# Optimization experiments

Measured on AMD Instinct MI355X. Metric: run time of the kernel, lower is better.

Reference implementation:

```python
import jax, jax.numpy as jnp
import numpy as np

B, N1, N2 = 4, 2048, 8192
F_IN, F_OUT = 256, 256
K = 3          # PyG knn_interpolate default
BN_EPS = 1e-5


def linear_bn(x, W, b, gamma, beta):
    # Linear + BatchNorm1d (training mode: batch stats over B*N per feature)
    h = jnp.einsum('bni,io->bno', x, W) + b
    mean = h.mean(axis=(0, 1))
    var = h.var(axis=(0, 1))
    xhat = (h - mean) * jax.lax.rsqrt(var + BN_EPS)
    return gamma * xhat + beta


def knn_interpolate(f1, p1, p2):
    # f1: [N1,F], p1: [N1,3], p2: [N2,3] -> [N2,F]
    d2 = jnp.sum((p2[:, None, :] - p1[None, :, :]) ** 2, axis=-1)  # [N2,N1]
    neg_d2, idx = jax.lax.top_k(-d2, K)                            # k smallest
    w = 1.0 / jnp.maximum(-neg_d2, 1e-16)                          # [N2,K]
    fk = f1[idx]                                                   # [N2,K,F]
    return jnp.sum(w[..., None] * fk, axis=1) / jnp.sum(w, axis=1, keepdims=True)


def setup_inputs() -> dict:
    key = jax.random.key(0)
    ks = jax.random.split(key, 10)
    return {
        'features_1': jax.random.normal(ks[0], (B, N1, F_IN), jnp.float32),
        'positions_1': jax.random.uniform(ks[1], (B, N1, 3), jnp.float32),
        'batch_1': jnp.repeat(jnp.arange(B, dtype=jnp.int64), N1),
        'features_2': jax.random.normal(ks[2], (B, N2, F_IN), jnp.float32),
        'positions_2': jax.random.uniform(ks[3], (B, N2, 3), jnp.float32),
        'batch_2': jnp.repeat(jnp.arange(B, dtype=jnp.int64), N2),
        'W1': jax.random.normal(ks[4], (F_IN, F_OUT), jnp.float32) * (1.0 / np.sqrt(F_IN)),
        'b1': jax.random.normal(ks[5], (F_OUT,), jnp.float32) * 0.02,
        'gamma1': jnp.ones((F_OUT,), jnp.float32),
        'beta1': jnp.zeros((F_OUT,), jnp.float32),
        'W2': jax.random.normal(ks[6], (F_IN, F_OUT), jnp.float32) * (1.0 / np.sqrt(F_IN)),
        'b2': jax.random.normal(ks[7], (F_OUT,), jnp.float32) * 0.02,
        'gamma2': jnp.ones((F_OUT,), jnp.float32),
        'beta2': jnp.zeros((F_OUT,), jnp.float32),
    }


def reference(features_1, positions_1, batch_1, features_2, positions_2, batch_2,
              W1, b1, gamma1, beta1, W2, b2, gamma2, beta2):
    f1 = linear_bn(features_1, W1, b1, gamma1, beta1)          # [B,N1,F_OUT]
    f2 = linear_bn(features_2, W2, b2, gamma2, beta2)          # [B,N2,F_OUT]
    # batch structure is regular [B,N]: knn restricted within batch == vmap over B
    interp = jax.vmap(knn_interpolate)(f1, positions_1, positions_2)  # [B,N2,F_OUT]
    return (interp + f2, positions_2, batch_2)
```

## Files before the change

### kernel.cpp

```cpp
#include <hip/hip_runtime.h>
#include <math.h>

#define BATCH   4
#define N1      2048
#define N2      8192
#define F       256
#define NTOT1   (BATCH * N1)
#define NTOT2   (BATCH * N2)
#define BN_EPS  1e-5f

typedef __attribute__((ext_vector_type(8))) short bf16x8;
typedef __attribute__((ext_vector_type(4))) float f32x4;

__device__ __forceinline__ unsigned short f2bf(float f) {
    unsigned u = __float_as_uint(f);
    unsigned r = (u + 0x7fffu + ((u >> 16) & 1u)) >> 16;
    return (unsigned short)r;
}
__device__ __forceinline__ float bf2f(unsigned short u) {
    return __uint_as_float((unsigned)u << 16);
}
__device__ __forceinline__ void async16(const void* g, void* l) {
    __builtin_amdgcn_global_load_lds(
        (const __attribute__((address_space(1))) unsigned int*)g,
        (__attribute__((address_space(3))) unsigned int*)l, 16, 0, 0);
}
__device__ __forceinline__ void ins3b(float d, int j,
                                      float& d0, float& d1, float& d2,
                                      int& j0, int& j1, int& j2) {
    const bool c0 = d < d0;
    const bool c1 = d < d1;
    const bool c2 = d < d2;
    d2 = c1 ? d1 : (c2 ? d : d2);
    j2 = c1 ? j1 : (c2 ? j : j2);
    d1 = c0 ? d0 : (c1 ? d : d1);
    j1 = c0 ? j0 : (c1 ? j : j1);
    d0 = c0 ? d  : d0;
    j0 = c0 ? j  : j0;
}

__global__ __launch_bounds__(256) void prep_kernel(const float4* __restrict__ f1,
                                                   const float4* __restrict__ f2,
                                                   const float* __restrict__ W1,
                                                   const float* __restrict__ W2,
                                                   ushort4* __restrict__ Xb1,
                                                   ushort4* __restrict__ Xb2,
                                                   unsigned short* __restrict__ Wt1,
                                                   unsigned short* __restrict__ Wt2,
                                                   float* __restrict__ sums) {
    const int bx = blockIdx.x;
    const int t  = threadIdx.x;

    if (bx < 8192) {
        const int i = bx * 256 + t;
        const float4 v = f2[i];
        ushort4 o;
        o.x = f2bf(v.x); o.y = f2bf(v.y); o.z = f2bf(v.z); o.w = f2bf(v.w);
        Xb2[i] = o;
    } else if (bx < 10240) {
        const int i = (bx - 8192) * 256 + t;
        const float4 v = f1[i];
        ushort4 o;
        o.x = f2bf(v.x); o.y = f2bf(v.y); o.z = f2bf(v.z); o.w = f2bf(v.w);
        Xb1[i] = o;
    } else if (bx < 10272) {
        __shared__ float tile[64][65];
        const int bb = bx - 10240;
        const bool second = bb >= 16;
        const int bl = second ? bb - 16 : bb;
        const float* W = second ? W2 : W1;
        unsigned short* Wt = second ? Wt2 : Wt1;
        const int gx0 = (bl & 3) * 64;
        const int gy0 = (bl >> 2) * 64;
        const int tx = t & 63;
        const int ty = t >> 6;
        #pragma unroll
        for (int j = 0; j < 16; ++j) {
            const int row = ty * 16 + j;
            tile[row][tx] = W[(size_t)(gy0 + row) * 256 + gx0 + tx];
        }
        __syncthreads();
        #pragma unroll
        for (int j = 0; j < 16; ++j) {
            const int row = ty * 16 + j;
            Wt[(size_t)(gx0 + row) * 256 + gy0 + tx] = f2bf(tile[tx][row]);
        }
    } else {
        #pragma unroll
        for (int i = 0; i < 4; ++i) sums[t + 256 * i] = 0.0f;
    }
}

__global__ __launch_bounds__(256) void gemm_mfma_kernel(const unsigned short* __restrict__ Xb1,
                                                        const unsigned short* __restrict__ Xb2,
                                                        const unsigned short* __restrict__ Wt1,
                                                        const unsigned short* __restrict__ Wt2,
                                                        const float* __restrict__ b1,
                                                        const float* __restrict__ b2,
                                                        unsigned short* __restrict__ h1b,
                                                        unsigned short* __restrict__ h2b,
                                                        float* __restrict__ sums) {
    __shared__ unsigned short As[128 * 32];
    __shared__ unsigned short Bs[128 * 32];

    const int bx   = blockIdx.x;
    const bool g2  = bx >= 64;
    const unsigned short* Xb = g2 ? Xb2 : Xb1;
    const unsigned short* Wt = g2 ? Wt2 : Wt1;
    const float* bias        = g2 ? b2 : b1;
    unsigned short* Hb       = g2 ? h2b : h1b;
    float* sum               = sums + (g2 ? 512 : 0);
    float* sumsq             = sum + 256;
    const int row0 = (g2 ? bx - 64 : bx) * 128;
    const int n0   = blockIdx.y * 128;

    const int t    = threadIdx.x;
    const int wave = t >> 6;
    const int lane = t & 63;
    const int wm   = (wave & 1) * 64;
    const int wn   = (wave >> 1) * 64;
    const int ml   = lane & 15;
    const int q    = lane >> 4;

    f32x4 acc[4][4] = {};

    for (int kt = 0; kt < 256; kt += 32) {
        #pragma unroll
        for (int r = 0; r < 2; ++r) {
            const int e   = r * 2048 + t * 8;
            const int row = e >> 5;
            const int kk  = e & 31;
            async16(Xb + (size_t)(row0 + row) * 256 + kt + kk, (unsigned short*)As + e);
            async16(Wt + (size_t)(n0 + row) * 256 + kt + kk, (unsigned short*)Bs + e);
        }
        __syncthreads();

        bf16x8 af[4], bfr[4];
        #pragma unroll
        for (int mt = 0; mt < 4; ++mt)
            af[mt] = *(const bf16x8*)&As[(wm + mt * 16 + ml) * 32 + q * 8];
        #pragma unroll
        for (int nt = 0; nt < 4; ++nt)
            bfr[nt] = *(const bf16x8*)&Bs[(wn + nt * 16 + ml) * 32 + q * 8];
        #pragma unroll
        for (int mt = 0; mt < 4; ++mt)
            #pragma unroll
            for (int nt = 0; nt < 4; ++nt)
                acc[mt][nt] = __builtin_amdgcn_mfma_f32_16x16x32_bf16(af[mt], bfr[nt],
                                                                      acc[mt][nt], 0, 0, 0);
        __syncthreads();
    }

    float bv[4], psum[4], psq[4];
    #pragma unroll
    for (int nt = 0; nt < 4; ++nt) {
        bv[nt] = bias[n0 + wn + nt * 16 + ml];
        psum[nt] = 0.0f; psq[nt] = 0.0f;
    }
    #pragma unroll
    for (int mt = 0; mt < 4; ++mt)
        #pragma unroll
        for (int nt = 0; nt < 4; ++nt)
            #pragma unroll
            for (int r = 0; r < 4; ++r) {
                const float v = acc[mt][nt][r] + bv[nt];
                const int grow = row0 + wm + mt * 16 + q * 4 + r;
                Hb[(size_t)grow * 256 + n0 + wn + nt * 16 + ml] = f2bf(v);
                psum[nt] += v;
                psq[nt]  = fmaf(v, v, psq[nt]);
            }
    #pragma unroll
    for (int nt = 0; nt < 4; ++nt) {
        psum[nt] += __shfl_xor(psum[nt], 16, 64);
        psum[nt] += __shfl_xor(psum[nt], 32, 64);
        psq[nt]  += __shfl_xor(psq[nt], 16, 64);
        psq[nt]  += __shfl_xor(psq[nt], 32, 64);
    }
    if (q == 0) {
        #pragma unroll
        for (int nt = 0; nt < 4; ++nt) {
            const int col = n0 + wn + nt * 16 + ml;
            atomicAdd(&sum[col],   psum[nt]);
            atomicAdd(&sumsq[col], psq[nt]);
        }
    }
}

__global__ __launch_bounds__(512) void fused_kernel(const float* __restrict__ p1,
                                                    const float* __restrict__ p2,
                                                    const unsigned short* __restrict__ h1b,
                                                    const unsigned short* __restrict__ h2b,
                                                    const float* __restrict__ sums,
                                                    const float* __restrict__ g1,
                                                    const float* __restrict__ be1,
                                                    const float* __restrict__ g2,
                                                    const float* __restrict__ be2,
                                                    float* __restrict__ out) {
    __shared__ float4 pts[N1];
    __shared__ float  pdl[8][128][3];
    __shared__ int    pil[8][128][3];
    __shared__ float  wql[128][3];
    __shared__ int    jql[128][3];
    __shared__ float  ssl[4][256];

    const int t     = threadIdx.x;
    const int bx    = blockIdx.x;
    const int qbase = bx * 128;
    const int b     = bx >> 6;
    const int wave  = t >> 6;
    const int lane  = t & 63;

    #pragma unroll
    for (int r = 0; r < 4; ++r) {
        const int j = t * 4 + r;
        const size_t base = (size_t)(b * N1 + j) * 3;
        pts[j] = make_float4(p1[base + 0], p1[base + 1], p1[base + 2], 0.0f);
    }
    if (t < 256) {
        const float m1 = sums[t] * (1.0f / (float)NTOT1);
        const float v1 = sums[256 + t] * (1.0f / (float)NTOT1) - m1 * m1;
        const float s1 = g1[t] * rsqrtf(v1 + BN_EPS);
        ssl[0][t] = s1;
        ssl[1][t] = be1[t] - m1 * s1;
        const float m2 = sums[512 + t] * (1.0f / (float)NTOT2);
        const float v2 = sums[768 + t] * (1.0f / (float)NTOT2) - m2 * m2;
        const float s2 = g2[t] * rsqrtf(v2 + BN_EPS);
        ssl[2][t] = s2;
        ssl[3][t] = be2[t] - m2 * s2;
    }
    __syncthreads();

    {
        const int iq0 = qbase + lane;
        const int iq1 = qbase + 64 + lane;
        const float qx0 = p2[(size_t)iq0 * 3 + 0];
        const float qy0 = p2[(size_t)iq0 * 3 + 1];
        const float qz0 = p2[(size_t)iq0 * 3 + 2];
        const float qx1 = p2[(size_t)iq1 * 3 + 0];
        const float qy1 = p2[(size_t)iq1 * 3 + 1];
        const float qz1 = p2[(size_t)iq1 * 3 + 2];

        float a0 = 1e30f, a1 = 1e30f, a2 = 1e30f; int ai0 = 0, ai1 = 0, ai2 = 0;
        float c0 = 1e30f, c1 = 1e30f, c2 = 1e30f; int ci0 = 0, ci1 = 0, ci2 = 0;

        const int jb = wave * 256;
        #pragma unroll 8
        for (int jj = 0; jj < 256; ++jj) {
            const float4 p = pts[jb + jj];
            {
                const float dx = p.x - qx0, dy = p.y - qy0, dz = p.z - qz0;
                float d = dx * dx; d = fmaf(dy, dy, d); d = fmaf(dz, dz, d);
                ins3b(d, jj, a0, a1, a2, ai0, ai1, ai2);
            }
            {
                const float dx = p.x - qx1, dy = p.y - qy1, dz = p.z - qz1;
                float d = dx * dx; d = fmaf(dy, dy, d); d = fmaf(dz, dz, d);
                ins3b(d, jj, c0, c1, c2, ci0, ci1, ci2);
            }
        }
        pdl[wave][lane][0] = a0; pdl[wave][lane][1] = a1; pdl[wave][lane][2] = a2;
        pil[wave][lane][0] = jb + ai0; pil[wave][lane][1] = jb + ai1; pil[wave][lane][2] = jb + ai2;
        pdl[wave][64 + lane][0] = c0; pdl[wave][64 + lane][1] = c1; pdl[wave][64 + lane][2] = c2;
        pil[wave][64 + lane][0] = jb + ci0; pil[wave][64 + lane][1] = jb + ci1; pil[wave][64 + lane][2] = jb + ci2;
    }
    __syncthreads();

    if (t < 128) {
        float d0 = 1e30f, d1 = 1e30f, d2 = 1e30f;
        int   j0 = 0,     j1 = 0,     j2 = 0;
        #pragma unroll
        for (int s = 0; s < 8; ++s)
            #pragma unroll
            for (int k = 0; k < 3; ++k)
                ins3b(pdl[s][t][k], pil[s][t][k], d0, d1, d2, j0, j1, j2);

        const float w0 = 1.0f / fmaxf(d0, 1e-16f);
        const float w1 = 1.0f / fmaxf(d1, 1e-16f);
        const float w2 = 1.0f / fmaxf(d2, 1e-16f);
        const float inv = 1.0f / (w0 + w1 + w2);
        wql[t][0] = w0 * inv; wql[t][1] = w1 * inv; wql[t][2] = w2 * inv;
        jql[t][0] = b * N1 + j0; jql[t][1] = b * N1 + j1; jql[t][2] = b * N1 + j2;
    }
    __syncthreads();

    {
        const int f    = t & 255;
        const int half = t >> 8;
        const float s1 = ssl[0][f], t1 = ssl[1][f];
        const float s2 = ssl[2][f], t2 = ssl[3][f];

        for (int qq = 0; qq < 64; ++qq) {
            const int v = half * 64 + qq;
            const int i = qbase + v;
            const int   j0 = jql[v][0], j1 = jql[v][1], j2 = jql[v][2];
            const float w0 = wql[v][0], w1 = wql[v][1], w2 = wql[v][2];

            float a = w0 * bf2f(h1b[(size_t)j0 * F + f]);
            a = fmaf(w1, bf2f(h1b[(size_t)j1 * F + f]), a);
            a = fmaf(w2, bf2f(h1b[(size_t)j2 * F + f]), a);
            const float h2v = bf2f(h2b[(size_t)i * F + f]);
            out[(size_t)i * F + f] = fmaf(a, s1, t1) + fmaf(h2v, s2, t2);
        }
    }

    {
        const int tid = bx * 512 + t;
        if (tid < NTOT2 * 3) {
            out[(size_t)NTOT2 * F + tid] = p2[tid];
        } else {
            const int e = tid - NTOT2 * 3;
            out[(size_t)NTOT2 * F + NTOT2 * 3 + e] = (float)(e >> 13);
        }
    }
}

extern "C" void kernel_launch(void* const* d_in, const int* in_sizes, int n_in,
                              void* d_out, int out_size, void* d_ws, size_t ws_size,
                              hipStream_t stream) {
    const float* f1  = (const float*)d_in[0];
    const float* p1  = (const float*)d_in[1];
    const float* f2  = (const float*)d_in[3];
    const float* p2  = (const float*)d_in[4];
    const float* W1  = (const float*)d_in[6];
    const float* b1  = (const float*)d_in[7];
    const float* g1  = (const float*)d_in[8];
    const float* be1 = (const float*)d_in[9];
    const float* W2  = (const float*)d_in[10];
    const float* b2  = (const float*)d_in[11];
    const float* g2  = (const float*)d_in[12];
    const float* be2 = (const float*)d_in[13];

    char* ws = (char*)d_ws;
    unsigned short* Xb1  = (unsigned short*)(ws);
    unsigned short* Xb2  = (unsigned short*)(ws + 4194304);
    unsigned short* Wt1  = (unsigned short*)(ws + 20971520);
    unsigned short* Wt2  = (unsigned short*)(ws + 21102592);
    unsigned short* h1b  = (unsigned short*)(ws + 21233664);
    unsigned short* h2b  = (unsigned short*)(ws + 25427968);
    float*          sums = (float*)(ws + 42205184);
    float*          out  = (float*)d_out;

    prep_kernel<<<10273, 256, 0, stream>>>((const float4*)f1, (const float4*)f2,
                                           W1, W2, (ushort4*)Xb1, (ushort4*)Xb2,
                                           Wt1, Wt2, sums);

    dim3 gg(320, 2);
    gemm_mfma_kernel<<<gg, 256, 0, stream>>>(Xb1, Xb2, Wt1, Wt2, b1, b2,
                                             h1b, h2b, sums);

    fused_kernel<<<256, 512, 0, stream>>>(p1, p2, h1b, h2b, sums,
                                          g1, be1, g2, be2, out);
}
```

Before: 196.1 us.

## Halve queries per block, SoA point layout, and vectorize bf16 gather pairs

The fused kNN kernel now handles 64 queries per block across 512 blocks instead of 128 across 256, so each lane tracks one query instead of two. Reference points are stored as separate x/y/z arrays in shared memory and read as float4 vectors, four candidates per load. The gather/output phase processes two features per thread with 32-bit bf16-pair loads and float2 stores. The aim is more blocks to fill the CUs and wider memory accesses. The cost is that each block reloads the full point set, so those loads double overall.

```diff
diff --git a/kernel.cpp b/kernel.cpp
--- a/kernel.cpp
+++ b/kernel.cpp
@@ -17,8 +17,11 @@
     unsigned r = (u + 0x7fffu + ((u >> 16) & 1u)) >> 16;
     return (unsigned short)r;
 }
-__device__ __forceinline__ float bf2f(unsigned short u) {
-    return __uint_as_float((unsigned)u << 16);
+__device__ __forceinline__ float bflo(unsigned u) {
+    return __uint_as_float(u << 16);
+}
+__device__ __forceinline__ float bfhi(unsigned u) {
+    return __uint_as_float(u & 0xffff0000u);
 }
 __device__ __forceinline__ void async16(const void* g, void* l) {
     __builtin_amdgcn_global_load_lds(
@@ -196,25 +199,27 @@
                                                     const float* __restrict__ g2,
                                                     const float* __restrict__ be2,
                                                     float* __restrict__ out) {
-    __shared__ float4 pts[N1];
-    __shared__ float  pdl[8][128][3];
-    __shared__ int    pil[8][128][3];
-    __shared__ float  wql[128][3];
-    __shared__ int    jql[128][3];
-    __shared__ float  ssl[4][256];
+    __shared__ float px[N1], py[N1], pz[N1];
+    __shared__ float pdl[8][64][3];
+    __shared__ int   pil[8][64][3];
+    __shared__ float wql[64][3];
+    __shared__ int   jql[64][3];
+    __shared__ float ssl[4][256];
 
     const int t     = threadIdx.x;
     const int bx    = blockIdx.x;
-    const int qbase = bx * 128;
-    const int b     = bx >> 6;
+    const int qbase = bx * 64;
+    const int b     = bx >> 7;
     const int wave  = t >> 6;
     const int lane  = t & 63;
 
     #pragma unroll
     for (int r = 0; r < 4; ++r) {
-        const int j = t * 4 + r;
+        const int j = r * 512 + t;
         const size_t base = (size_t)(b * N1 + j) * 3;
-        pts[j] = make_float4(p1[base + 0], p1[base + 1], p1[base + 2], 0.0f);
+        px[j] = p1[base + 0];
+        py[j] = p1[base + 1];
+        pz[j] = p1[base + 2];
     }
     if (t < 256) {
         const float m1 = sums[t] * (1.0f / (float)NTOT1);
@@ -231,41 +236,47 @@
     __syncthreads();
 
     {
-        const int iq0 = qbase + lane;
-        const int iq1 = qbase + 64 + lane;
-        const float qx0 = p2[(size_t)iq0 * 3 + 0];
-        const float qy0 = p2[(size_t)iq0 * 3 + 1];
-        const float qz0 = p2[(size_t)iq0 * 3 + 2];
-        const float qx1 = p2[(size_t)iq1 * 3 + 0];
-        const float qy1 = p2[(size_t)iq1 * 3 + 1];
-        const float qz1 = p2[(size_t)iq1 * 3 + 2];
-
-        float a0 = 1e30f, a1 = 1e30f, a2 = 1e30f; int ai0 = 0, ai1 = 0, ai2 = 0;
-        float c0 = 1e30f, c1 = 1e30f, c2 = 1e30f; int ci0 = 0, ci1 = 0, ci2 = 0;
+        const int iq = qbase + lane;
+        const float qx = p2[(size_t)iq * 3 + 0];
+        const float qy = p2[(size_t)iq * 3 + 1];
+        const float qz = p2[(size_t)iq * 3 + 2];
+
+        float d0 = 1e30f, d1 = 1e30f, d2 = 1e30f;
+        int   i0 = 0,     i1 = 0,     i2 = 0;
 
         const int jb = wave * 256;
-        #pragma unroll 8
-        for (int jj = 0; jj < 256; ++jj) {
-            const float4 p = pts[jb + jj];
+        #pragma unroll 2
+        for (int jj = 0; jj < 256; jj += 4) {
+            const float4 x4 = *(const float4*)&px[jb + jj];
+            const float4 y4 = *(const float4*)&py[jb + jj];
+            const float4 z4 = *(const float4*)&pz[jb + jj];
             {
-                const float dx = p.x - qx0, dy = p.y - qy0, dz = p.z - qz0;
+                const float dx = x4.x - qx, dy = y4.x - qy, dz = z4.x - qz;
                 float d = dx * dx; d = fmaf(dy, dy, d); d = fmaf(dz, dz, d);
-                ins3b(d, jj, a0, a1, a2, ai0, ai1, ai2);
+                ins3b(d, jj + 0, d0, d1, d2, i0, i1, i2);
             }
             {
-                const float dx = p.x - qx1, dy = p.y - qy1, dz = p.z - qz1;
+                const float dx = x4.y - qx, dy = y4.y - qy, dz = z4.y - qz;
                 float d = dx * dx; d = fmaf(dy, dy, d); d = fmaf(dz, dz, d);
-                ins3b(d, jj, c0, c1, c2, ci0, ci1, ci2);
-            }
-        }
-        pdl[wave][lane][0] = a0; pdl[wave][lane][1] = a1; pdl[wave][lane][2] = a2;
-        pil[wave][lane][0] = jb + ai0; pil[wave][lane][1] = jb + ai1; pil[wave][lane][2] = jb + ai2;
-        pdl[wave][64 + lane][0] = c0; pdl[wave][64 + lane][1] = c1; pdl[wave][64 + lane][2] = c2;
-        pil[wave][64 + lane][0] = jb + ci0; pil[wave][64 + lane][1] = jb + ci1; pil[wave][64 + lane][2] = jb + ci2;
+                ins3b(d, jj + 1, d0, d1, d2, i0, i1, i2);
+            }
+            {
+                const float dx = x4.z - qx, dy = y4.z - qy, dz = z4.z - qz;
+                float d = dx * dx; d = fmaf(dy, dy, d); d = fmaf(dz, dz, d);
+                ins3b(d, jj + 2, d0, d1, d2, i0, i1, i2);
+            }
+            {
+                const float dx = x4.w - qx, dy = y4.w - qy, dz = z4.w - qz;
+                float d = dx * dx; d = fmaf(dy, dy, d); d = fmaf(dz, dz, d);
+                ins3b(d, jj + 3, d0, d1, d2, i0, i1, i2);
+            }
+        }
+        pdl[wave][lane][0] = d0; pdl[wave][lane][1] = d1; pdl[wave][lane][2] = d2;
+        pil[wave][lane][0] = jb + i0; pil[wave][lane][1] = jb + i1; pil[wave][lane][2] = jb + i2;
     }
     __syncthreads();
 
-    if (t < 128) {
+    if (t < 64) {
         float d0 = 1e30f, d1 = 1e30f, d2 = 1e30f;
         int   j0 = 0,     j1 = 0,     j2 = 0;
         #pragma unroll
@@ -284,27 +295,41 @@
     __syncthreads();
 
     {
-        const int f    = t & 255;
-        const int half = t >> 8;
-        const float s1 = ssl[0][f], t1 = ssl[1][f];
-        const float s2 = ssl[2][f], t2 = ssl[3][f];
-
-        for (int qq = 0; qq < 64; ++qq) {
-            const int v = half * 64 + qq;
+        const int fp = t & 127;
+        const int f0 = fp * 2;
+        const int qg = t >> 7;
+        const float s1a = ssl[0][f0], t1a = ssl[1][f0];
+        const float s2a = ssl[2][f0], t2a = ssl[3][f0];
+        const float s1b = ssl[0][f0 + 1], t1b = ssl[1][f0 + 1];
+        const float s2b = ssl[2][f0 + 1], t2b = ssl[3][f0 + 1];
+
+        for (int qq = 0; qq < 16; ++qq) {
+            const int v = qg * 16 + qq;
             const int i = qbase + v;
             const int   j0 = jql[v][0], j1 = jql[v][1], j2 = jql[v][2];
             const float w0 = wql[v][0], w1 = wql[v][1], w2 = wql[v][2];
 
-            float a = w0 * bf2f(h1b[(size_t)j0 * F + f]);
-            a = fmaf(w1, bf2f(h1b[(size_t)j1 * F + f]), a);
-            a = fmaf(w2, bf2f(h1b[(size_t)j2 * F + f]), a);
-            const float h2v = bf2f(h2b[(size_t)i * F + f]);
-            out[(size_t)i * F + f] = fmaf(a, s1, t1) + fmaf(h2v, s2, t2);
-        }
-    }
-
-    {
-        const int tid = bx * 512 + t;
+            const unsigned u0 = *(const unsigned*)(h1b + (size_t)j0 * F + f0);
+            const unsigned u1 = *(const unsigned*)(h1b + (size_t)j1 * F + f0);
+            const unsigned u2 = *(const unsigned*)(h1b + (size_t)j2 * F + f0);
+            const unsigned uh = *(const unsigned*)(h2b + (size_t)i * F + f0);
+
+            float alo = w0 * bflo(u0);
+            alo = fmaf(w1, bflo(u1), alo);
+            alo = fmaf(w2, bflo(u2), alo);
+            float ahi = w0 * bfhi(u0);
+            ahi = fmaf(w1, bfhi(u1), ahi);
+            ahi = fmaf(w2, bfhi(u2), ahi);
+
+            float2 o;
+            o.x = fmaf(alo, s1a, t1a) + fmaf(bflo(uh), s2a, t2a);
+            o.y = fmaf(ahi, s1b, t1b) + fmaf(bfhi(uh), s2b, t2b);
+            *(float2*)(out + (size_t)i * F + f0) = o;
+        }
+    }
+
+    if (t < 256) {
+        const int tid = bx * 256 + t;
         if (tid < NTOT2 * 3) {
             out[(size_t)NTOT2 * F + tid] = p2[tid];
         } else {
@@ -348,6 +373,6 @@
     gemm_mfma_kernel<<<gg, 256, 0, stream>>>(Xb1, Xb2, Wt1, Wt2, b1, b2,
                                              h1b, h2b, sums);
 
-    fused_kernel<<<256, 512, 0, stream>>>(p1, p2, h1b, h2b, sums,
+    fused_kernel<<<512, 512, 0, stream>>>(p1, p2, h1b, h2b, sums,
                                           g1, be1, g2, be2, out);
 }
```

Result: faster. 185.4 us (-5.4%).
